# Kernel optimization log

Hardware: AMD Instinct MI355X
Metric: run time of the kernel (lower is better)

The kernel has to match this reference:

```python
import jax, jax.numpy as jnp
import numpy as np

B, N, H = 4, 4096, 1024
NH, HD, M = 16, 64, 256
EPS = 1e-5


def gaussian_orthogonal(m, d, rng):
    # scaling=0: rows are orthogonal blocks scaled by norms of fresh gaussian rows
    blocks = []
    n_blocks = (m + d - 1) // d
    for _ in range(n_blocks):
        q, _ = np.linalg.qr(rng.standard_normal((d, d)))
        blocks.append(q.T)
    mat = np.concatenate(blocks, 0)[:m]
    multiplier = np.linalg.norm(rng.standard_normal((m, d)), axis=1)
    return (multiplier[:, None] * mat).astype(np.float32)


def setup_inputs():
    key = jax.random.key(0)
    keys = iter(jax.random.split(key, 24))
    rng = np.random.default_rng(0)

    def w(din, dout):
        return jax.random.normal(next(keys), (din, dout), jnp.float32) * 0.02

    inp = {
        'x': jax.random.normal(next(keys), (B, N, H), jnp.float32),
        'enc_outputs': jax.random.normal(next(keys), (B, N, H), jnp.float32),
    }
    for p in ('sa', 'ca'):
        for q in ('wq', 'wk', 'wv', 'wo'):
            inp[f'{p}_{q}'] = w(H, H)
            inp[f'{p}_b{q[1]}'] = jnp.zeros((H,), jnp.float32)
        inp[f'{p}_proj'] = jnp.asarray(gaussian_orthogonal(M, HD, rng))
    inp['ff_w1'] = w(H, 4 * H); inp['ff_b1'] = jnp.zeros((4 * H,), jnp.float32)
    inp['ff_w2'] = w(4 * H, H); inp['ff_b2'] = jnp.zeros((H,), jnp.float32)
    for i in (1, 2, 3):
        inp[f'ln{i}_g'] = jnp.ones((H,), jnp.float32)
        inp[f'ln{i}_b'] = jnp.zeros((H,), jnp.float32)
    return inp


def _split(t):
    b, n, _ = t.shape
    return t.reshape(b, n, NH, HD).transpose(0, 2, 1, 3)  # [b,h,n,d]


def _feat(data, proj):
    # FAVOR+ nonnegative softmax kernel features
    dn = HD ** -0.25
    dd = jnp.einsum('bhnd,md->bhnm', data * dn, proj)
    diag = 0.5 * (dn ** 2) * jnp.sum(data * data, -1)  # [b,h,n]
    dd = dd - diag[..., None] - jnp.max(dd, axis=-1, keepdims=True)
    return (M ** -0.5) * (jnp.exp(dd) + 1e-4)


def _attn(q, k, v, wq, bq, wk, bk, wv, bv, wo, bo, proj):
    b, n, _ = q.shape
    Q = _split(q @ wq + bq)
    K = _split(k @ wk + bk)
    V = _split(v @ wv + bv)
    Qp = _feat(Q, proj)  # [b,h,n,m]
    Kp = _feat(K, proj)
    denom = jnp.einsum('bhnm,bhm->bhn', Qp, Kp.sum(2))[..., None]
    ctx = jnp.einsum('bhnm,bhnd->bhmd', Kp, V)          # O(N) linear attention
    out = jnp.einsum('bhnm,bhmd->bhnd', Qp, ctx) / denom
    # faithful to torch .view(B,-1,hidden) WITHOUT head transpose-back
    out = out.reshape(b, -1, H)
    return out @ wo + bo


def _ln(x, g, b):
    mu = jnp.mean(x, -1, keepdims=True)
    var = jnp.mean((x - mu) ** 2, -1, keepdims=True)
    return (x - mu) / jnp.sqrt(var + EPS) * g + b


def reference(x, enc_outputs, sa_wq, sa_bq, sa_wk, sa_bk, sa_wv, sa_bv, sa_wo, sa_bo,
              sa_proj, ca_wq, ca_bq, ca_wk, ca_bk, ca_wv, ca_bv, ca_wo, ca_bo, ca_proj,
              ff_w1, ff_b1, ff_w2, ff_b2, ln1_g, ln1_b, ln2_g, ln2_b, ln3_g, ln3_b):
    h = _ln(x + _attn(x, x, x, sa_wq, sa_bq, sa_wk, sa_bk, sa_wv, sa_bv, sa_wo, sa_bo, sa_proj), ln1_g, ln1_b)
    h = _ln(h + _attn(h, enc_outputs, enc_outputs, ca_wq, ca_bq, ca_wk, ca_bk, ca_wv, ca_bv, ca_wo, ca_bo, ca_proj), ln2_g, ln2_b)
    ff = jax.nn.gelu(h @ ff_w1 + ff_b1, approximate=True) @ ff_w2 + ff_b2  # dropout prob 0 -> identity
    return _ln(h + ff, ln3_g, ln3_b)
```

## Files before the change

### kernel.cpp

```cpp
#include <hip/hip_runtime.h>
#include <hip/hip_bf16.h>

#define B_ 4
#define N_ 4096
#define H_ 1024
#define NH_ 16
#define HD_ 64
#define M_ 256

typedef __attribute__((ext_vector_type(8))) __bf16 bf16x8;
typedef __attribute__((ext_vector_type(4))) float f32x4;
typedef __attribute__((ext_vector_type(4))) unsigned int u32x4;

__device__ __forceinline__ float bf2f(unsigned short u) {
  union { unsigned int i; float f; } x; x.i = ((unsigned int)u) << 16; return x.f;
}
__device__ __forceinline__ unsigned short f2b(float f) {
  __hip_bfloat16 h = __float2bfloat16(f);
  return *(unsigned short*)&h;
}
__device__ __forceinline__ float gelu_f(float x) {
  const float c = 0.7978845608028654f;
  float t = tanhf(c * (x + 0.044715f * x * x * x));
  return 0.5f * x * (1.0f + t);
}

typedef __attribute__((address_space(3))) unsigned int as3_uint;
typedef const __attribute__((address_space(1))) unsigned int as1_uint;
__device__ __forceinline__ void gload16(const void* g, void* l) {
  __builtin_amdgcn_global_load_lds((as1_uint*)g, (as3_uint*)l, 16, 0, 0);
}

template<int ACT>
__launch_bounds__(256)
__global__ void gemm_mfma(const unsigned short* __restrict__ A, int lda,
                          const unsigned short* __restrict__ BT,
                          const float* __restrict__ bias,
                          unsigned short* __restrict__ C, int ldc, int K) {
  __shared__ __align__(16) char LDS[65536];

  const int tid = threadIdx.x;
  const int nwg = gridDim.x * gridDim.y;
  const int lin = blockIdx.y * gridDim.x + blockIdx.x;
  const int mm = (lin & 7) * (nwg >> 3) + (lin >> 3);
  const int bx = mm % gridDim.x, by = mm / gridDim.x;
  const int row0 = by * 128;
  const int col0 = bx * 128;

  const int w = tid >> 6, lane = tid & 63;
  const int wm = w >> 1, wn = w & 1;
  const int ln = lane & 15, hi = lane >> 4;
  const int rswz = (ln & 7) << 4;

  const int srow = w * 8 + (lane >> 3);
  const int schunk = ((lane & 7) ^ (lane >> 3)) * 8;
  const unsigned short* Ag = A + (long long)(row0 + srow) * lda + schunk;
  const unsigned short* Bg = BT + (long long)(col0 + srow) * K + schunk;
  const int ldsw = w * 1024;

  f32x4 acc[4][4];
#pragma unroll
  for (int i = 0; i < 4; ++i)
#pragma unroll
    for (int j = 0; j < 4; ++j) acc[i][j] = (f32x4){0.f, 0.f, 0.f, 0.f};

  auto STAGE = [&](int p, int k0) {
    char* dst = LDS + p * 32768 + ldsw;
#pragma unroll
    for (int i = 0; i < 4; ++i) {
      gload16(Ag + (long long)i * 32 * lda + k0, dst + i * 4096);
      gload16(Bg + (long long)i * 32 * K + k0, dst + 16384 + i * 4096);
    }
  };
  auto COMPUTE = [&](int p) {
    char* AsB = LDS + p * 32768;
    char* BsB = AsB + 16384;
#pragma unroll
    for (int kc = 0; kc < 2; ++kc) {
      const int koff = (kc * 64 + hi * 16) ^ rswz;
      bf16x8 av[4], bv[4];
#pragma unroll
      for (int i = 0; i < 4; ++i)
        av[i] = *(bf16x8*)(AsB + (wm * 64 + i * 16 + ln) * 128 + koff);
#pragma unroll
      for (int j = 0; j < 4; ++j)
        bv[j] = *(bf16x8*)(BsB + (wn * 64 + j * 16 + ln) * 128 + koff);
#pragma unroll
      for (int i = 0; i < 4; ++i)
#pragma unroll
        for (int j = 0; j < 4; ++j)
          acc[i][j] = __builtin_amdgcn_mfma_f32_16x16x32_bf16(av[i], bv[j], acc[i][j], 0, 0, 0);
    }
  };

  STAGE(0, 0);
  __syncthreads();
  int cur = 0;
  for (int k0 = 64; k0 < K; k0 += 64) {
    STAGE(cur ^ 1, k0);
    COMPUTE(cur);
    __syncthreads();
    cur ^= 1;
  }
  COMPUTE(cur);
  __syncthreads();

  char* SB = LDS;
#pragma unroll
  for (int j = 0; j < 4; ++j) {
    const int lcol = wn * 64 + j * 16 + ln;
    const float bj = bias ? bias[col0 + lcol] : 0.0f;
#pragma unroll
    for (int i = 0; i < 4; ++i) {
      const int rb_ = wm * 64 + i * 16 + hi * 4;
#pragma unroll
      for (int r = 0; r < 4; ++r) {
        float v = acc[i][j][r] + bj;
        if (ACT == 1) v = gelu_f(v);
        const int row = rb_ + r;
        *(unsigned short*)(SB + ((row * 256 + lcol * 2) ^ ((row & 7) << 4))) = f2b(v);
      }
    }
  }
  __syncthreads();
#pragma unroll
  for (int p = 0; p < 8; ++p) {
    const int idx = p * 256 + tid;
    const int row = idx >> 4, seg = idx & 15;
    u32x4 v = *(u32x4*)(SB + ((row * 256 + seg * 16) ^ ((row & 7) << 4)));
    __builtin_nontemporal_store(v, (u32x4*)(C + (long long)(row0 + row) * ldc + col0 + seg * 8));
  }
}

__launch_bounds__(256)
__global__ void ctxksum_mfma(const unsigned short* __restrict__ QKV,
                             const unsigned short* __restrict__ pjB,
                             float* __restrict__ ksum,
                             float* __restrict__ ctxA) {
  __shared__ char Kt[8192];
  __shared__ char Vt[8192];
  __shared__ char Pt[32768];
  __shared__ float rmaxL[4][64];
  __shared__ float ssqL[64];
  const int z = blockIdx.z, b = z >> 4, hh = z & 15;
  const int n0 = blockIdx.x * 512;
  const unsigned short* Kg = QKV + (long long)(b * 4096) * 3072 + 1024 + hh * 64;
  const unsigned short* Vg = QKV + (long long)(b * 4096) * 3072 + 2048 + hh * 64;
  const int tid = threadIdx.x;
  const int w = tid >> 6, lane = tid & 63;
  const int ln = lane & 15, hi = lane >> 4;
  const int rswz = (ln & 7) << 4;

  f32x4 accC[4][4];
#pragma unroll
  for (int i = 0; i < 4; ++i)
#pragma unroll
    for (int j = 0; j < 4; ++j) accC[i][j] = (f32x4){0.f, 0.f, 0.f, 0.f};
  float cs[4] = {0.f, 0.f, 0.f, 0.f};

  for (int t = 0; t < 8; ++t) {
    const long long nt = n0 + t * 64;
    __syncthreads();
#pragma unroll
    for (int p = 0; p < 2; ++p) {
      int id = p * 256 + tid;
      int r = id >> 3, c = id & 7;
      gload16(Kg + (nt + r) * 3072 + ((c ^ (r & 7)) * 8), Kt + id * 16);
    }
    {
      int n = tid >> 2, d0 = (tid & 3) * 16;
      const unsigned short* src = Vg + (nt + n) * 3072 + d0;
      ushort4 v0 = *(const ushort4*)src;
      ushort4 v1 = *(const ushort4*)(src + 4);
      ushort4 v2 = *(const ushort4*)(src + 8);
      ushort4 v3 = *(const ushort4*)(src + 12);
      unsigned short vals[16] = {v0.x, v0.y, v0.z, v0.w, v1.x, v1.y, v1.z, v1.w,
                                 v2.x, v2.y, v2.z, v2.w, v3.x, v3.y, v3.z, v3.w};
#pragma unroll
      for (int e = 0; e < 16; ++e) {
        int d = d0 + e;
        *(unsigned short*)(Vt + ((d * 128 + n * 2) ^ ((d & 7) << 4))) = vals[e];
      }
    }
    __syncthreads();

    f32x4 accF[4][4];
#pragma unroll
    for (int i = 0; i < 4; ++i)
#pragma unroll
      for (int j = 0; j < 4; ++j) accF[i][j] = (f32x4){0.f, 0.f, 0.f, 0.f};
#pragma unroll
    for (int kc = 0; kc < 2; ++kc) {
      const int koff = (kc * 64 + hi * 16) ^ rswz;
      bf16x8 av[4], bq[4];
#pragma unroll
      for (int i = 0; i < 4; ++i)
        av[i] = *(bf16x8*)(Kt + (i * 16 + ln) * 128 + koff);
#pragma unroll
      for (int j = 0; j < 4; ++j)
        bq[j] = *(const bf16x8*)(pjB + (w * 64 + j * 16 + ln) * 64 + kc * 32 + hi * 8);
#pragma unroll
      for (int i = 0; i < 4; ++i)
#pragma unroll
        for (int j = 0; j < 4; ++j)
          accF[i][j] = __builtin_amdgcn_mfma_f32_16x16x32_bf16(av[i], bq[j], accF[i][j], 0, 0, 0);
    }

#pragma unroll
    for (int i = 0; i < 4; ++i)
#pragma unroll
      for (int r = 0; r < 4; ++r) {
        float m = fmaxf(fmaxf(accF[i][0][r], accF[i][1][r]), fmaxf(accF[i][2][r], accF[i][3][r]));
        m = fmaxf(m, __shfl_xor(m, 1, 64));
        m = fmaxf(m, __shfl_xor(m, 2, 64));
        m = fmaxf(m, __shfl_xor(m, 4, 64));
        m = fmaxf(m, __shfl_xor(m, 8, 64));
        if (ln == 0) rmaxL[w][i * 16 + hi * 4 + r] = m;
      }
    {
      int r = tid >> 2, q = tid & 3;
      int b0 = (r * 128 + q * 32) ^ ((r & 7) << 4);
      int b1 = (r * 128 + q * 32 + 16) ^ ((r & 7) << 4);
      u32x4 x0 = *(u32x4*)(Kt + b0);
      u32x4 x1 = *(u32x4*)(Kt + b1);
      float s = 0.f;
#pragma unroll
      for (int e = 0; e < 4; ++e) {
        float a0 = bf2f((unsigned short)(x0[e] & 0xffff)), a1 = bf2f((unsigned short)(x0[e] >> 16));
        float a2 = bf2f((unsigned short)(x1[e] & 0xffff)), a3 = bf2f((unsigned short)(x1[e] >> 16));
        s += a0 * a0 + a1 * a1 + a2 * a2 + a3 * a3;
      }
      s += __shfl_xor(s, 1, 64);
      s += __shfl_xor(s, 2, 64);
      if (q == 0) ssqL[r] = s;
    }
    __syncthreads();

    float base[4][4];
#pragma unroll
    for (int i = 0; i < 4; ++i)
#pragma unroll
      for (int r = 0; r < 4; ++r) {
        int row = i * 16 + hi * 4 + r;
        base[i][r] = 0.0625f * ssqL[row] +
                     fmaxf(fmaxf(rmaxL[0][row], rmaxL[1][row]), fmaxf(rmaxL[2][row], rmaxL[3][row]));
      }
#pragma unroll
    for (int i = 0; i < 4; ++i)
#pragma unroll
      for (int j = 0; j < 4; ++j) {
        ushort4 pk;
        float v0 = 0.0625f * (expf(accF[i][j][0] - base[i][0]) + 1e-4f);
        float v1 = 0.0625f * (expf(accF[i][j][1] - base[i][1]) + 1e-4f);
        float v2 = 0.0625f * (expf(accF[i][j][2] - base[i][2]) + 1e-4f);
        float v3 = 0.0625f * (expf(accF[i][j][3] - base[i][3]) + 1e-4f);
        cs[j] += v0 + v1 + v2 + v3;
        pk.x = f2b(v0); pk.y = f2b(v1); pk.z = f2b(v2); pk.w = f2b(v3);
        int m = w * 64 + j * 16 + ln;
        *(ushort4*)(Pt + ((m * 128 + i * 32 + hi * 8) ^ ((m & 7) << 4))) = pk;
      }
    __syncthreads();

#pragma unroll
    for (int kc = 0; kc < 2; ++kc) {
      const int koff = (kc * 64 + hi * 16) ^ rswz;
      bf16x8 am[4], bv[4];
#pragma unroll
      for (int i = 0; i < 4; ++i)
        am[i] = *(bf16x8*)(Pt + (w * 64 + i * 16 + ln) * 128 + koff);
#pragma unroll
      for (int j = 0; j < 4; ++j)
        bv[j] = *(bf16x8*)(Vt + (j * 16 + ln) * 128 + koff);
#pragma unroll
      for (int i = 0; i < 4; ++i)
#pragma unroll
        for (int j = 0; j < 4; ++j)
          accC[i][j] = __builtin_amdgcn_mfma_f32_16x16x32_bf16(am[i], bv[j], accC[i][j], 0, 0, 0);
    }
  }

#pragma unroll
  for (int j = 0; j < 4; ++j) {
    cs[j] += __shfl_xor(cs[j], 16, 64);
    cs[j] += __shfl_xor(cs[j], 32, 64);
  }
  if (hi == 0) {
#pragma unroll
    for (int j = 0; j < 4; ++j)
      atomicAdd(&ksum[z * 256 + w * 64 + j * 16 + ln], cs[j]);
  }
#pragma unroll
  for (int i = 0; i < 4; ++i)
#pragma unroll
    for (int j = 0; j < 4; ++j)
#pragma unroll
      for (int r = 0; r < 4; ++r)
        atomicAdd(&ctxA[(long long)z * 16384 + (w * 64 + i * 16 + hi * 4 + r) * 64 + j * 16 + ln],
                  accC[i][j][r]);
}

__launch_bounds__(256)
__global__ void ctx_fin(const float* __restrict__ ctxA, unsigned short* __restrict__ ctxbf) {
  const int z = blockIdx.x;
  const float* src = ctxA + (long long)z * 16384;
  unsigned short* dst = ctxbf + (long long)z * 16384;
  for (int cc = threadIdx.x; cc < 2048; cc += 256) {
    int mh = cc >> 10, rem = cc & 1023, d = rem >> 4, cl = rem & 15;
    int m0 = mh * 128 + cl * 8;
    ushort4 o0, o1;
    o0.x = f2b(src[(m0 + 0) * 64 + d]); o0.y = f2b(src[(m0 + 1) * 64 + d]);
    o0.z = f2b(src[(m0 + 2) * 64 + d]); o0.w = f2b(src[(m0 + 3) * 64 + d]);
    o1.x = f2b(src[(m0 + 4) * 64 + d]); o1.y = f2b(src[(m0 + 5) * 64 + d]);
    o1.z = f2b(src[(m0 + 6) * 64 + d]); o1.w = f2b(src[(m0 + 7) * 64 + d]);
    unsigned short* p = dst + (long long)mh * 8192 + (d * 16 + (cl ^ (d & 7))) * 8;
    *(ushort4*)p = o0;
    *(ushort4*)(p + 4) = o1;
  }
}

__launch_bounds__(256)
__global__ void ao_fused(const unsigned short* __restrict__ QKV,
                         const unsigned short* __restrict__ pjB,
                         const float* __restrict__ ksum,
                         const unsigned short* __restrict__ ctxbf,
                         unsigned short* __restrict__ AO) {
  __shared__ char Qt[8192];
  __shared__ char Ps[32768];
  __shared__ char Ch[16384];
  __shared__ float rmaxL[4][64];
  __shared__ float ssqL[64];
  __shared__ float dprt[4][64];
  __shared__ float denomS[64];
  const int z = blockIdx.z, b = z >> 4, hh = z & 15;
  const int n0 = blockIdx.x * 64;
  const unsigned short* Qg = QKV + (long long)(b * 4096) * 3072 + hh * 64;
  const int tid = threadIdx.x;
  const int w = tid >> 6, lane = tid & 63;
  const int ln = lane & 15, hi = lane >> 4;
  const int rswz = (ln & 7) << 4;

#pragma unroll
  for (int p = 0; p < 2; ++p) {
    int id = p * 256 + tid;
    int r = id >> 3, c = id & 7;
    gload16(Qg + (long long)(n0 + r) * 3072 + ((c ^ (r & 7)) * 8), Qt + id * 16);
  }
  __syncthreads();

  f32x4 accF[4][4];
#pragma unroll
  for (int i = 0; i < 4; ++i)
#pragma unroll
    for (int j = 0; j < 4; ++j) accF[i][j] = (f32x4){0.f, 0.f, 0.f, 0.f};
#pragma unroll
  for (int kc = 0; kc < 2; ++kc) {
    const int koff = (kc * 64 + hi * 16) ^ rswz;
    bf16x8 av[4], bq[4];
#pragma unroll
    for (int i = 0; i < 4; ++i)
      av[i] = *(bf16x8*)(Qt + (i * 16 + ln) * 128 + koff);
#pragma unroll
    for (int j = 0; j < 4; ++j)
      bq[j] = *(const bf16x8*)(pjB + (w * 64 + j * 16 + ln) * 64 + kc * 32 + hi * 8);
#pragma unroll
    for (int i = 0; i < 4; ++i)
#pragma unroll
      for (int j = 0; j < 4; ++j)
        accF[i][j] = __builtin_amdgcn_mfma_f32_16x16x32_bf16(av[i], bq[j], accF[i][j], 0, 0, 0);
  }

#pragma unroll
  for (int i = 0; i < 4; ++i)
#pragma unroll
    for (int r = 0; r < 4; ++r) {
      float m = fmaxf(fmaxf(accF[i][0][r], accF[i][1][r]), fmaxf(accF[i][2][r], accF[i][3][r]));
      m = fmaxf(m, __shfl_xor(m, 1, 64));
      m = fmaxf(m, __shfl_xor(m, 2, 64));
      m = fmaxf(m, __shfl_xor(m, 4, 64));
      m = fmaxf(m, __shfl_xor(m, 8, 64));
      if (ln == 0) rmaxL[w][i * 16 + hi * 4 + r] = m;
    }
  {
    int r = tid >> 2, q = tid & 3;
    int b0 = (r * 128 + q * 32) ^ ((r & 7) << 4);
    int b1 = (r * 128 + q * 32 + 16) ^ ((r & 7) << 4);
    u32x4 x0 = *(u32x4*)(Qt + b0);
    u32x4 x1 = *(u32x4*)(Qt + b1);
    float s = 0.f;
#pragma unroll
    for (int e = 0; e < 4; ++e) {
      float a0 = bf2f((unsigned short)(x0[e] & 0xffff)), a1 = bf2f((unsigned short)(x0[e] >> 16));
      float a2 = bf2f((unsigned short)(x1[e] & 0xffff)), a3 = bf2f((unsigned short)(x1[e] >> 16));
      s += a0 * a0 + a1 * a1 + a2 * a2 + a3 * a3;
    }
    s += __shfl_xor(s, 1, 64);
    s += __shfl_xor(s, 2, 64);
    if (q == 0) ssqL[r] = s;
  }
  __syncthreads();

  float ks[4];
#pragma unroll
  for (int j = 0; j < 4; ++j) ks[j] = ksum[z * 256 + w * 64 + j * 16 + ln];
#pragma unroll
  for (int i = 0; i < 4; ++i)
#pragma unroll
    for (int r = 0; r < 4; ++r) {
      int n = i * 16 + hi * 4 + r;
      float base = 0.0625f * ssqL[n] +
                   fmaxf(fmaxf(rmaxL[0][n], rmaxL[1][n]), fmaxf(rmaxL[2][n], rmaxL[3][n]));
      float dp = 0.f;
#pragma unroll
      for (int j = 0; j < 4; ++j) {
        float v = 0.0625f * (expf(accF[i][j][r] - base) + 1e-4f);
        int m = w * 64 + j * 16 + ln;
        *(unsigned short*)(Ps + n * 512 + ((m * 2) ^ ((n & 7) << 4))) = f2b(v);
        dp += v * ks[j];
      }
      dp += __shfl_xor(dp, 1, 64);
      dp += __shfl_xor(dp, 2, 64);
      dp += __shfl_xor(dp, 4, 64);
      dp += __shfl_xor(dp, 8, 64);
      if (ln == 0) dprt[w][n] = dp;
    }
  __syncthreads();
  if (tid < 64) denomS[tid] = dprt[0][tid] + dprt[1][tid] + dprt[2][tid] + dprt[3][tid];

  f32x4 accO[4];
#pragma unroll
  for (int j = 0; j < 4; ++j) accO[j] = (f32x4){0.f, 0.f, 0.f, 0.f};
#pragma unroll
  for (int mh = 0; mh < 2; ++mh) {
#pragma unroll
    for (int p = 0; p < 4; ++p) {
      int id = p * 256 + tid;
      gload16(ctxbf + (long long)z * 16384 + mh * 8192 + id * 8, Ch + id * 16);
    }
    __syncthreads();
#pragma unroll
    for (int ms = 0; ms < 4; ++ms) {
      const int koff = (ms * 64 + hi * 16);
      bf16x8 ap = *(bf16x8*)(Ps + (w * 16 + ln) * 512 + ((mh * 256 + koff) ^ rswz));
      bf16x8 bc[4];
#pragma unroll
      for (int j = 0; j < 4; ++j)
        bc[j] = *(bf16x8*)(Ch + (j * 16 + ln) * 256 + (koff ^ rswz));
#pragma unroll
      for (int j = 0; j < 4; ++j)
        accO[j] = __builtin_amdgcn_mfma_f32_16x16x32_bf16(ap, bc[j], accO[j], 0, 0, 0);
    }
    __syncthreads();
  }

  float inv[4];
#pragma unroll
  for (int r = 0; r < 4; ++r) inv[r] = 1.0f / denomS[w * 16 + hi * 4 + r];
  char* Ct = Qt;
#pragma unroll
  for (int j = 0; j < 4; ++j)
#pragma unroll
    for (int r = 0; r < 4; ++r) {
      int n = w * 16 + hi * 4 + r;
      int d = j * 16 + ln;
      *(unsigned short*)(Ct + ((n * 128 + d * 2) ^ ((n & 7) << 4))) = f2b(accO[j][r] * inv[r]);
    }
  __syncthreads();
#pragma unroll
  for (int p = 0; p < 2; ++p) {
    int idx = p * 256 + tid;
    int row = idx >> 3, seg = idx & 7;
    u32x4 v = *(u32x4*)(Ct + ((row * 128 + seg * 16) ^ ((row & 7) << 4)));
    *(u32x4*)(AO + (long long)(b * 4096 + n0 + row) * 1024 + hh * 64 + seg * 8) = v;
  }
}

__launch_bounds__(256)
__global__ void wt_cvt(const float* __restrict__ in, unsigned short* __restrict__ out,
                       int K, int N) {
  __shared__ float t[32][33];
  int k0 = blockIdx.y * 32, n0 = blockIdx.x * 32;
  int tx = threadIdx.x & 31, ty = threadIdx.x >> 5;
  for (int r = ty; r < 32; r += 8) t[r][tx] = in[(long long)(k0 + r) * N + n0 + tx];
  __syncthreads();
  for (int r = ty; r < 32; r += 8) out[(long long)(n0 + r) * K + k0 + tx] = f2b(t[tx][r]);
}

__launch_bounds__(256)
__global__ void projB_cvt(const float* __restrict__ proj, unsigned short* __restrict__ out) {
  int i = blockIdx.x * 256 + threadIdx.x;
  out[i] = f2b(0.35355339059327373f * proj[i]);
}

__launch_bounds__(256)
__global__ void bias_cat(const float* __restrict__ b0, const float* __restrict__ b1,
                         const float* __restrict__ b2, float* __restrict__ out) {
  int i = blockIdx.x * 256 + threadIdx.x;
  float v;
  if (i < 1024) v = b0[i];
  else if (i < 2048) v = b1[i - 1024];
  else v = b2[i - 2048];
  out[i] = v;
}

__launch_bounds__(256)
__global__ void cvt_bf16(const float* __restrict__ in, unsigned short* __restrict__ out,
                         long long n) {
  long long stride = (long long)gridDim.x * 1024;
  for (long long i = ((long long)blockIdx.x * 256 + threadIdx.x) * 4; i < n; i += stride) {
    float4 v = *(const float4*)&in[i];
    ushort4 o;
    o.x = f2b(v.x); o.y = f2b(v.y); o.z = f2b(v.z); o.w = f2b(v.w);
    *(ushort4*)&out[i] = o;
  }
}

__launch_bounds__(256)
__global__ void ln_k(const float* __restrict__ resf, const unsigned short* __restrict__ resb,
                     const unsigned short* __restrict__ po,
                     const float* __restrict__ g, const float* __restrict__ be,
                     float* __restrict__ outf, unsigned short* __restrict__ outb) {
  long long row = blockIdx.x;
  int t = threadIdx.x;
  float x0, x1, x2, x3;
  if (resf) {
    float4 va = ((const float4*)(resf + row * H_))[t];
    x0 = va.x; x1 = va.y; x2 = va.z; x3 = va.w;
  } else {
    ushort4 va = ((const ushort4*)(resb + row * H_))[t];
    x0 = bf2f(va.x); x1 = bf2f(va.y); x2 = bf2f(va.z); x3 = bf2f(va.w);
  }
  {
    ushort4 vp = ((const ushort4*)(po + row * H_))[t];
    x0 += bf2f(vp.x); x1 += bf2f(vp.y); x2 += bf2f(vp.z); x3 += bf2f(vp.w);
  }
  float s = x0 + x1 + x2 + x3;
  float q = x0 * x0 + x1 * x1 + x2 * x2 + x3 * x3;
#pragma unroll
  for (int m = 1; m < 64; m <<= 1) { s += __shfl_xor(s, m, 64); q += __shfl_xor(q, m, 64); }
  __shared__ float ssum[4], ssq[4];
  int w = t >> 6, lane = t & 63;
  if (lane == 0) { ssum[w] = s; ssq[w] = q; }
  __syncthreads();
  s = ssum[0] + ssum[1] + ssum[2] + ssum[3];
  q = ssq[0] + ssq[1] + ssq[2] + ssq[3];
  float mean = s * (1.0f / H_);
  float var = q * (1.0f / H_) - mean * mean;
  float rstd = rsqrtf(var + 1e-5f);
  float4 vg = ((const float4*)g)[t];
  float4 vbe = ((const float4*)be)[t];
  float o0 = (x0 - mean) * rstd * vg.x + vbe.x;
  float o1 = (x1 - mean) * rstd * vg.y + vbe.y;
  float o2 = (x2 - mean) * rstd * vg.z + vbe.z;
  float o3 = (x3 - mean) * rstd * vg.w + vbe.w;
  if (outf) {
    float4 o; o.x = o0; o.y = o1; o.z = o2; o.w = o3;
    ((float4*)(outf + row * H_))[t] = o;
  }
  if (outb) {
    ushort4 ob; ob.x = f2b(o0); ob.y = f2b(o1); ob.z = f2b(o2); ob.w = f2b(o3);
    ((ushort4*)(outb + row * H_))[t] = ob;
  }
}

extern "C" void kernel_launch(void* const* d_in, const int* in_sizes, int n_in,
                              void* d_out, int out_size, void* d_ws, size_t ws_size,
                              hipStream_t stream) {
  (void)in_sizes; (void)n_in; (void)out_size; (void)ws_size;
  const float* x      = (const float*)d_in[0];
  const float* enc    = (const float*)d_in[1];
  const float* sa_w[4] = {(const float*)d_in[2], (const float*)d_in[4], (const float*)d_in[6], (const float*)d_in[8]};
  const float* sa_b[4] = {(const float*)d_in[3], (const float*)d_in[5], (const float*)d_in[7], (const float*)d_in[9]};
  const float* sa_pj  = (const float*)d_in[10];
  const float* ca_w[4] = {(const float*)d_in[11], (const float*)d_in[13], (const float*)d_in[15], (const float*)d_in[17]};
  const float* ca_b[4] = {(const float*)d_in[12], (const float*)d_in[14], (const float*)d_in[16], (const float*)d_in[18]};
  const float* ca_pj  = (const float*)d_in[19];
  const float* ff_w1  = (const float*)d_in[20];
  const float* ff_b1  = (const float*)d_in[21];
  const float* ff_w2  = (const float*)d_in[22];
  const float* ff_b2  = (const float*)d_in[23];
  const float* ln1_g  = (const float*)d_in[24];
  const float* ln1_b  = (const float*)d_in[25];
  const float* ln2_g  = (const float*)d_in[26];
  const float* ln2_b  = (const float*)d_in[27];
  const float* ln3_g  = (const float*)d_in[28];
  const float* ln3_b  = (const float*)d_in[29];

  float* ws = (float*)d_ws;
  unsigned short* XB = (unsigned short*)(ws);
  unsigned short* EB = (unsigned short*)(ws + 8388608LL);
  unsigned short* QKVb = (unsigned short*)(ws + 16777216LL);
  unsigned short* PO = (unsigned short*)(ws + 41943040LL);
  unsigned short* MIDB = PO;
  unsigned short* FO = (unsigned short*)(ws + 50331648LL);
  unsigned short* WTph = (unsigned short*)(ws + 52428800LL);
  unsigned short* pjB = (unsigned short*)(ws + 54525952LL);
  float* ctxA  = ws + 54542336LL;
  float* ksumA = ws + 55590912LL;
  unsigned short* ctxbf = (unsigned short*)(ws + 55607296LL);
  float* biasC = ws + 56131584LL;

  unsigned short* ff1T = EB;
  unsigned short* ff2T = EB + 4194304LL;
  unsigned short* pjB_sa = pjB, *pjB_ca = pjB + 16384;

  dim3 blk(256, 1, 1);
  const int LDQ = 3072;

  projB_cvt<<<dim3(64), blk, 0, stream>>>(sa_pj, pjB_sa);
  projB_cvt<<<dim3(64), blk, 0, stream>>>(ca_pj, pjB_ca);
  cvt_bf16<<<dim3(2048), blk, 0, stream>>>(x, XB, 16777216LL);

  auto attn_core = [&](const unsigned short* pj, const float* wo_bias) {
    hipMemsetAsync(ctxA, 0, (1048576LL + 16384LL) * sizeof(float), stream);
    ctxksum_mfma<<<dim3(8, 1, 64), blk, 0, stream>>>(QKVb, pj, ksumA, ctxA);
    ctx_fin<<<dim3(64), blk, 0, stream>>>(ctxA, ctxbf);
    ao_fused<<<dim3(64, 1, 64), blk, 0, stream>>>(QKVb, pj, ksumA, ctxbf, EB);
    gemm_mfma<0><<<dim3(8, 128), blk, 0, stream>>>(EB, H_, WTph + 3145728, wo_bias, PO, H_, H_);
  };

  for (int i = 0; i < 4; ++i)
    wt_cvt<<<dim3(32, 32), blk, 0, stream>>>(sa_w[i], WTph + (long long)i * 1048576, H_, H_);
  bias_cat<<<dim3(12), blk, 0, stream>>>(sa_b[0], sa_b[1], sa_b[2], biasC);
  gemm_mfma<0><<<dim3(24, 128), blk, 0, stream>>>(XB, H_, WTph, biasC, QKVb, LDQ, H_);
  attn_core(pjB_sa, sa_b[3]);
  ln_k<<<dim3(16384), blk, 0, stream>>>(x, nullptr, PO, ln1_g, ln1_b, nullptr, XB);

  cvt_bf16<<<dim3(2048), blk, 0, stream>>>(enc, EB, 16777216LL);
  for (int i = 0; i < 4; ++i)
    wt_cvt<<<dim3(32, 32), blk, 0, stream>>>(ca_w[i], WTph + (long long)i * 1048576, H_, H_);
  bias_cat<<<dim3(8), blk, 0, stream>>>(ca_b[1], ca_b[2], nullptr, biasC);
  gemm_mfma<0><<<dim3(8, 128), blk, 0, stream>>>(XB, H_, WTph, ca_b[0], QKVb, LDQ, H_);
  gemm_mfma<0><<<dim3(16, 128), blk, 0, stream>>>(EB, H_, WTph + 1048576, biasC, QKVb + 1024, LDQ, H_);
  attn_core(pjB_ca, ca_b[3]);
  ln_k<<<dim3(16384), blk, 0, stream>>>(nullptr, XB, PO, ln2_g, ln2_b, nullptr, XB);

  wt_cvt<<<dim3(128, 32), blk, 0, stream>>>(ff_w1, ff1T, H_, 4096);
  wt_cvt<<<dim3(32, 128), blk, 0, stream>>>(ff_w2, ff2T, 4096, H_);
  for (int c = 0; c < 4; ++c) {
    const long long co = (long long)c * 4096 * H_;
    gemm_mfma<1><<<dim3(32, 32), blk, 0, stream>>>(XB + co, H_, ff1T, ff_b1, MIDB, 4096, H_);
    gemm_mfma<0><<<dim3(8, 32), blk, 0, stream>>>(MIDB, 4096, ff2T, ff_b2, FO, H_, 4096);
    ln_k<<<dim3(4096), blk, 0, stream>>>(nullptr, XB + co, FO, ln3_g, ln3_b,
                                         (float*)d_out + co, nullptr);
  }
}
```

Baseline: 1.543 ms.

## Replace atomic context accumulation with per-split partials and deterministic reduction

The context/ksum kernel now writes per-split partial sums through LDS-staged coalesced nontemporal stores instead of many scalar float atomics, and no longer needs a memset. ctx_fin reduces the eight partials in shared memory and also produces the final ksum. ao_fused prefetches the whole bf16 context into a doubled LDS buffer up front, which removes per-half barriers but raises LDS use and may lower occupancy. Feature and denominator sums now use bf16-rounded values so they match the stored probabilities.

```diff
diff --git a/kernel.cpp b/kernel.cpp
--- a/kernel.cpp
+++ b/kernel.cpp
@@ -135,15 +135,16 @@
 __launch_bounds__(256)
 __global__ void ctxksum_mfma(const unsigned short* __restrict__ QKV,
                              const unsigned short* __restrict__ pjB,
-                             float* __restrict__ ksum,
-                             float* __restrict__ ctxA) {
+                             float* __restrict__ ksumP,
+                             float* __restrict__ ctxP) {
   __shared__ char Kt[8192];
   __shared__ char Vt[8192];
   __shared__ char Pt[32768];
   __shared__ float rmaxL[4][64];
   __shared__ float ssqL[64];
   const int z = blockIdx.z, b = z >> 4, hh = z & 15;
-  const int n0 = blockIdx.x * 512;
+  const int sp = blockIdx.x;
+  const int n0 = sp * 512;
   const unsigned short* Kg = QKV + (long long)(b * 4096) * 3072 + 1024 + hh * 64;
   const unsigned short* Vg = QKV + (long long)(b * 4096) * 3072 + 2048 + hh * 64;
   const int tid = threadIdx.x;
@@ -250,12 +251,11 @@
 #pragma unroll
       for (int j = 0; j < 4; ++j) {
         ushort4 pk;
-        float v0 = 0.0625f * (expf(accF[i][j][0] - base[i][0]) + 1e-4f);
-        float v1 = 0.0625f * (expf(accF[i][j][1] - base[i][1]) + 1e-4f);
-        float v2 = 0.0625f * (expf(accF[i][j][2] - base[i][2]) + 1e-4f);
-        float v3 = 0.0625f * (expf(accF[i][j][3] - base[i][3]) + 1e-4f);
-        cs[j] += v0 + v1 + v2 + v3;
-        pk.x = f2b(v0); pk.y = f2b(v1); pk.z = f2b(v2); pk.w = f2b(v3);
+        pk.x = f2b(0.0625f * (expf(accF[i][j][0] - base[i][0]) + 1e-4f));
+        pk.y = f2b(0.0625f * (expf(accF[i][j][1] - base[i][1]) + 1e-4f));
+        pk.z = f2b(0.0625f * (expf(accF[i][j][2] - base[i][2]) + 1e-4f));
+        pk.w = f2b(0.0625f * (expf(accF[i][j][3] - base[i][3]) + 1e-4f));
+        cs[j] += bf2f(pk.x) + bf2f(pk.y) + bf2f(pk.z) + bf2f(pk.w);
         int m = w * 64 + j * 16 + ln;
         *(ushort4*)(Pt + ((m * 128 + i * 32 + hi * 8) ^ ((m & 7) << 4))) = pk;
       }
@@ -287,31 +287,71 @@
   if (hi == 0) {
 #pragma unroll
     for (int j = 0; j < 4; ++j)
-      atomicAdd(&ksum[z * 256 + w * 64 + j * 16 + ln], cs[j]);
-  }
-#pragma unroll
-  for (int i = 0; i < 4; ++i)
-#pragma unroll
-    for (int j = 0; j < 4; ++j)
-#pragma unroll
-      for (int r = 0; r < 4; ++r)
-        atomicAdd(&ctxA[(long long)z * 16384 + (w * 64 + i * 16 + hi * 4 + r) * 64 + j * 16 + ln],
-                  accC[i][j][r]);
-}
-
-__launch_bounds__(256)
-__global__ void ctx_fin(const float* __restrict__ ctxA, unsigned short* __restrict__ ctxbf) {
+      ksumP[((long long)z * 8 + sp) * 256 + w * 64 + j * 16 + ln] = cs[j];
+  }
+
+  float* ctxPs = ctxP + ((long long)z * 8 + sp) * 16384;
+#pragma unroll
+  for (int dh = 0; dh < 2; ++dh) {
+    __syncthreads();
+#pragma unroll
+    for (int i = 0; i < 4; ++i)
+#pragma unroll
+      for (int jj = 0; jj < 2; ++jj) {
+        int j = dh * 2 + jj;
+#pragma unroll
+        for (int r = 0; r < 4; ++r) {
+          int m = w * 64 + i * 16 + hi * 4 + r;
+          int dl = jj * 16 + ln;
+          *(float*)(Pt + ((m * 128 + dl * 4) ^ ((m & 7) << 4))) = accC[i][j][r];
+        }
+      }
+    __syncthreads();
+#pragma unroll
+    for (int p = 0; p < 8; ++p) {
+      int idx = p * 256 + tid;
+      int row = idx >> 3, seg = idx & 7;
+      u32x4 v = *(u32x4*)(Pt + ((row * 128 + seg * 16) ^ ((row & 7) << 4)));
+      __builtin_nontemporal_store(v, (u32x4*)(ctxPs + dh * 8192 + row * 32 + seg * 4));
+    }
+  }
+}
+
+__launch_bounds__(256)
+__global__ void ctx_fin(const float* __restrict__ ctxP, const float* __restrict__ ksumP,
+                        unsigned short* __restrict__ ctxbf, float* __restrict__ ksumF) {
+  __shared__ float acc[16384];
   const int z = blockIdx.x;
-  const float* src = ctxA + (long long)z * 16384;
+  const int tid = threadIdx.x;
+  const float* base = ctxP + (long long)z * 8 * 16384;
+  for (int i = tid; i < 16384; i += 256) {
+    float s = 0.f;
+#pragma unroll
+    for (int q = 0; q < 8; ++q) s += base[(long long)q * 16384 + i];
+    acc[i] = s;
+  }
+  {
+    const float* kb = ksumP + (long long)z * 8 * 256;
+    float s = 0.f;
+#pragma unroll
+    for (int q = 0; q < 8; ++q) s += kb[q * 256 + tid];
+    ksumF[z * 256 + tid] = s;
+  }
+  __syncthreads();
   unsigned short* dst = ctxbf + (long long)z * 16384;
-  for (int cc = threadIdx.x; cc < 2048; cc += 256) {
+  for (int cc = tid; cc < 2048; cc += 256) {
     int mh = cc >> 10, rem = cc & 1023, d = rem >> 4, cl = rem & 15;
     int m0 = mh * 128 + cl * 8;
+    int dh = d >> 5, dl = d & 31;
     ushort4 o0, o1;
-    o0.x = f2b(src[(m0 + 0) * 64 + d]); o0.y = f2b(src[(m0 + 1) * 64 + d]);
-    o0.z = f2b(src[(m0 + 2) * 64 + d]); o0.w = f2b(src[(m0 + 3) * 64 + d]);
-    o1.x = f2b(src[(m0 + 4) * 64 + d]); o1.y = f2b(src[(m0 + 5) * 64 + d]);
-    o1.z = f2b(src[(m0 + 6) * 64 + d]); o1.w = f2b(src[(m0 + 7) * 64 + d]);
+    o0.x = f2b(acc[dh * 8192 + (m0 + 0) * 32 + dl]);
+    o0.y = f2b(acc[dh * 8192 + (m0 + 1) * 32 + dl]);
+    o0.z = f2b(acc[dh * 8192 + (m0 + 2) * 32 + dl]);
+    o0.w = f2b(acc[dh * 8192 + (m0 + 3) * 32 + dl]);
+    o1.x = f2b(acc[dh * 8192 + (m0 + 4) * 32 + dl]);
+    o1.y = f2b(acc[dh * 8192 + (m0 + 5) * 32 + dl]);
+    o1.z = f2b(acc[dh * 8192 + (m0 + 6) * 32 + dl]);
+    o1.w = f2b(acc[dh * 8192 + (m0 + 7) * 32 + dl]);
     unsigned short* p = dst + (long long)mh * 8192 + (d * 16 + (cl ^ (d & 7))) * 8;
     *(ushort4*)p = o0;
     *(ushort4*)(p + 4) = o1;
@@ -326,7 +366,7 @@
                          unsigned short* __restrict__ AO) {
   __shared__ char Qt[8192];
   __shared__ char Ps[32768];
-  __shared__ char Ch[16384];
+  __shared__ char Ch[32768];
   __shared__ float rmaxL[4][64];
   __shared__ float ssqL[64];
   __shared__ float dprt[4][64];
@@ -340,6 +380,11 @@
   const int rswz = (ln & 7) << 4;
 
 #pragma unroll
+  for (int p = 0; p < 8; ++p) {
+    int id = p * 256 + tid;
+    gload16(ctxbf + (long long)z * 16384 + id * 8, Ch + id * 16);
+  }
+#pragma unroll
   for (int p = 0; p < 2; ++p) {
     int id = p * 256 + tid;
     int r = id >> 3, c = id & 7;
@@ -413,9 +458,10 @@
 #pragma unroll
       for (int j = 0; j < 4; ++j) {
         float v = 0.0625f * (expf(accF[i][j][r] - base) + 1e-4f);
+        unsigned short vb = f2b(v);
         int m = w * 64 + j * 16 + ln;
-        *(unsigned short*)(Ps + n * 512 + ((m * 2) ^ ((n & 7) << 4))) = f2b(v);
-        dp += v * ks[j];
+        *(unsigned short*)(Ps + n * 512 + ((m * 2) ^ ((n & 7) << 4))) = vb;
+        dp += bf2f(vb) * ks[j];
       }
       dp += __shfl_xor(dp, 1, 64);
       dp += __shfl_xor(dp, 2, 64);
@@ -432,25 +478,19 @@
 #pragma unroll
   for (int mh = 0; mh < 2; ++mh) {
 #pragma unroll
-    for (int p = 0; p < 4; ++p) {
-      int id = p * 256 + tid;
-      gload16(ctxbf + (long long)z * 16384 + mh * 8192 + id * 8, Ch + id * 16);
-    }
-    __syncthreads();
-#pragma unroll
     for (int ms = 0; ms < 4; ++ms) {
       const int koff = (ms * 64 + hi * 16);
       bf16x8 ap = *(bf16x8*)(Ps + (w * 16 + ln) * 512 + ((mh * 256 + koff) ^ rswz));
       bf16x8 bc[4];
 #pragma unroll
       for (int j = 0; j < 4; ++j)
-        bc[j] = *(bf16x8*)(Ch + (j * 16 + ln) * 256 + (koff ^ rswz));
+        bc[j] = *(bf16x8*)(Ch + mh * 16384 + (j * 16 + ln) * 256 + (koff ^ rswz));
 #pragma unroll
       for (int j = 0; j < 4; ++j)
         accO[j] = __builtin_amdgcn_mfma_f32_16x16x32_bf16(ap, bc[j], accO[j], 0, 0, 0);
     }
-    __syncthreads();
-  }
+  }
+  __syncthreads();
 
   float inv[4];
 #pragma unroll
@@ -590,12 +630,13 @@
   unsigned short* EB = (unsigned short*)(ws + 8388608LL);
   unsigned short* QKVb = (unsigned short*)(ws + 16777216LL);
   unsigned short* PO = (unsigned short*)(ws + 41943040LL);
+  float* ctxP = ws + 41943040LL;
   unsigned short* MIDB = PO;
   unsigned short* FO = (unsigned short*)(ws + 50331648LL);
   unsigned short* WTph = (unsigned short*)(ws + 52428800LL);
   unsigned short* pjB = (unsigned short*)(ws + 54525952LL);
-  float* ctxA  = ws + 54542336LL;
-  float* ksumA = ws + 55590912LL;
+  float* ksumP = ws + 54542336LL;
+  float* ksumF = ws + 54673408LL;
   unsigned short* ctxbf = (unsigned short*)(ws + 55607296LL);
   float* biasC = ws + 56131584LL;
 
@@ -611,10 +652,9 @@
   cvt_bf16<<<dim3(2048), blk, 0, stream>>>(x, XB, 16777216LL);
 
   auto attn_core = [&](const unsigned short* pj, const float* wo_bias) {
-    hipMemsetAsync(ctxA, 0, (1048576LL + 16384LL) * sizeof(float), stream);
-    ctxksum_mfma<<<dim3(8, 1, 64), blk, 0, stream>>>(QKVb, pj, ksumA, ctxA);
-    ctx_fin<<<dim3(64), blk, 0, stream>>>(ctxA, ctxbf);
-    ao_fused<<<dim3(64, 1, 64), blk, 0, stream>>>(QKVb, pj, ksumA, ctxbf, EB);
+    ctxksum_mfma<<<dim3(8, 1, 64), blk, 0, stream>>>(QKVb, pj, ksumP, ctxP);
+    ctx_fin<<<dim3(64), blk, 0, stream>>>(ctxP, ksumP, ctxbf, ksumF);
+    ao_fused<<<dim3(64, 1, 64), blk, 0, stream>>>(QKVb, pj, ksumF, ctxbf, EB);
     gemm_mfma<0><<<dim3(8, 128), blk, 0, stream>>>(EB, H_, WTph + 3145728, wo_bias, PO, H_, H_);
   };
 
```

Result: no change. 1.533 ms (-0.6%).
